# Optimization experiments

Hardware: AMD Instinct MI355X
Metric: run time of the kernel (lower is better)

The kernel has to match this reference:

```python
import jax, jax.numpy as jnp
import numpy as np

B, T, D = 32, 4096, 512  # batch, encoder timesteps t_k, attn_sz (== encoder dim == state_sz)


def setup_inputs() -> dict:
    key = jax.random.key(0)
    ks = jax.random.split(key, 7)
    scale = 1.0 / np.sqrt(D)
    return {
        "h_i": jax.random.normal(ks[0], (B, T, D), dtype=jnp.float32),
        "s_t": jax.random.normal(ks[1], (B, D), dtype=jnp.float32),
        "coverage": jax.random.uniform(ks[2], (B, T), dtype=jnp.float32),
        "W_h": jax.random.normal(ks[3], (D, D), dtype=jnp.float32) * scale,
        "W_s": jax.random.normal(ks[4], (D, D), dtype=jnp.float32) * scale,
        "b_s": jnp.zeros((D,), dtype=jnp.float32),
        "W_c": jax.random.normal(ks[5], (1, D), dtype=jnp.float32) * scale,
        "V": jax.random.normal(ks[6], (D, 1), dtype=jnp.float32) * scale,
    }


def reference(h_i, s_t, coverage, W_h, W_s, b_s, W_c, V):
    # enc_features: (B, T, D)
    enc_features = jnp.einsum("btd,de->bte", h_i, W_h)
    # dec_features: (B, D) broadcast over T
    dec_features = s_t @ W_s + b_s
    # coverage term: Dense(D) applied to coverage[..., None] -> outer product with W_c row
    cov_features = coverage[..., None] * W_c[0]  # (B, T, D)
    features = enc_features + dec_features[:, None, :] + cov_features
    # e_t = V(tanh(features)) squeezed to (B, T)
    e_t = jnp.einsum("bte,e->bt", jnp.tanh(features), V[:, 0])
    a_t = jax.nn.softmax(e_t, axis=1)  # (B, T)
    new_coverage = coverage + a_t
    # context = a_t^T h_i : (B, D)
    context_vector = jnp.einsum("bt,btd->bd", a_t, h_i)
    return context_vector, a_t, new_coverage
```

## Files before the change

### kernel.cpp

```cpp
#include <hip/hip_runtime.h>
#include <stdint.h>

#define B_ 32
#define T_ 4096
#define D_ 512
#define BT_ (B_*T_)

typedef __attribute__((ext_vector_type(8))) short bf16x8;
typedef __attribute__((ext_vector_type(4))) float f32x4;

__device__ __forceinline__ unsigned short f2bf(float f) {
    unsigned int u = __float_as_uint(f);
    u += 0x7FFFu + ((u >> 16) & 1u);
    return (unsigned short)(u >> 16);
}

__device__ __forceinline__ float tanh_fast(float x) {
    float e2 = __expf(2.0f * x);
    return 1.0f - 2.0f / (e2 + 1.0f);
}

__global__ __launch_bounds__(256) void k_conv_wh(const float* __restrict__ W_h,
                                                 unsigned short* __restrict__ wsb) {
    int tid = blockIdx.x * 256 + threadIdx.x;
    int l  = tid & 63;
    int kt = (tid >> 6) & 15;
    int nt = tid >> 10;
    int n  = nt * 16 + (l & 15);
    int k0 = kt * 32 + (l >> 4) * 8;
    unsigned int w[4];
#pragma unroll
    for (int q = 0; q < 4; ++q) {
        unsigned short lo = f2bf(W_h[(size_t)(k0 + 2*q)     * D_ + n]);
        unsigned short hi = f2bf(W_h[(size_t)(k0 + 2*q + 1) * D_ + n]);
        w[q] = (unsigned int)lo | ((unsigned int)hi << 16);
    }
    uint4 pk = {w[0], w[1], w[2], w[3]};
    ((uint4*)wsb)[tid] = pk;
}

__global__ __launch_bounds__(256) void k_dec(const float* __restrict__ s_t,
                                             const float* __restrict__ W_s,
                                             const float* __restrict__ b_s,
                                             float* __restrict__ dec) {
    int b = blockIdx.x;
    int c = threadIdx.x;
    float a0 = b_s[c], a1 = b_s[c + 256];
    const float* srow = s_t + b * D_;
    for (int k = 0; k < D_; ++k) {
        float s = srow[k];
        const float* wr = W_s + (size_t)k * D_;
        a0 = fmaf(s, wr[c], a0);
        a1 = fmaf(s, wr[c + 256], a1);
    }
    dec[b * D_ + c] = a0;
    dec[b * D_ + c + 256] = a1;
}

__global__ __launch_bounds__(512, 4) void k_main(const float* __restrict__ h_i,
                                                 const float* __restrict__ coverage,
                                                 const unsigned short* __restrict__ wsb,
                                                 const float* __restrict__ dec,
                                                 const float* __restrict__ W_c,
                                                 const float* __restrict__ V,
                                                 float* __restrict__ e_out,
                                                 float* __restrict__ part) {
    __shared__ __align__(16) unsigned char As[65536];
    __shared__ float red[8][64];
    __shared__ float wexp[64];
    const int tid = threadIdx.x;
    const int w = tid >> 6, l = tid & 63;
    const int row0 = blockIdx.x * 64;
    const int b    = row0 >> 12;
    const int t0   = row0 & (T_ - 1);

    float4 L0[8], L1[8];
#pragma unroll
    for (int i = 0; i < 8; ++i) {
        const float* src = h_i + (size_t)(row0 + i * 8 + w) * D_ + l * 8;
        L0[i] = *(const float4*)(src);
        L1[i] = *(const float4*)(src + 4);
    }
    {
        const int kt   = l >> 2;
        const int lam  = 16 * (l & 3);
        const int sl_m = (l & 3) << 1;
#pragma unroll
        for (int i = 0; i < 8; ++i) {
            int row = i * 8 + w;
            uint4 pk;
            pk.x = (unsigned)f2bf(L0[i].x) | ((unsigned)f2bf(L0[i].y) << 16);
            pk.y = (unsigned)f2bf(L0[i].z) | ((unsigned)f2bf(L0[i].w) << 16);
            pk.z = (unsigned)f2bf(L1[i].x) | ((unsigned)f2bf(L1[i].y) << 16);
            pk.w = (unsigned)f2bf(L1[i].z) | ((unsigned)f2bf(L1[i].w) << 16);
            int lamf = lam + (row & 15);
            int slot = (lamf & 0x38) | ((lamf & 7) ^ sl_m ^ (kt & 1));
            int byte = (((row >> 4) * 16 + kt) << 10) + (slot << 4);
            *(uint4*)(As + byte) = pk;
        }
    }
    __syncthreads();

    const int slotR = (l & 0x38) | ((l & 7) ^ (((l >> 4) & 3) << 1));

    f32x4 acc[4][4];
#pragma unroll
    for (int af = 0; af < 4; ++af)
#pragma unroll
        for (int j = 0; j < 4; ++j) acc[af][j] = (f32x4){0, 0, 0, 0};

    const uint4* bw = (const uint4*)wsb + ((w * 4) << 10) + l;

    {
        uint4 bp[2][4];
#pragma unroll
        for (int j = 0; j < 4; ++j) bp[0][j] = bw[(j << 10)];
#pragma unroll
        for (int j = 0; j < 4; ++j) bp[1][j] = bw[(j << 10) + (1 << 6)];
#pragma unroll
        for (int kt = 0; kt < 16; ++kt) {
            const int sl = ((slotR ^ (kt & 1)) << 4);
#pragma unroll
            for (int af = 0; af < 4; ++af) {
                uint4 araw = *(const uint4*)(As + ((af * 16 + kt) << 10) + sl);
                bf16x8 a = __builtin_bit_cast(bf16x8, araw);
#pragma unroll
                for (int j = 0; j < 4; ++j) {
                    bf16x8 bv = __builtin_bit_cast(bf16x8, bp[kt & 1][j]);
                    acc[af][j] = __builtin_amdgcn_mfma_f32_16x16x32_bf16(a, bv, acc[af][j], 0, 0, 0);
                }
            }
            if (kt < 14) {
#pragma unroll
                for (int j = 0; j < 4; ++j)
                    bp[kt & 1][j] = bw[(j << 10) + ((kt + 2) << 6)];
            }
        }
    }

    const int rgrp = (l >> 4) * 4;
    float cov_r[4][4];
#pragma unroll
    for (int af = 0; af < 4; ++af)
#pragma unroll
        for (int r = 0; r < 4; ++r)
            cov_r[af][r] = coverage[b * T_ + t0 + af * 16 + rgrp + r];

    float p[4][4] = {{0,0,0,0},{0,0,0,0},{0,0,0,0},{0,0,0,0}};
#pragma unroll
    for (int j = 0; j < 4; ++j) {
        int col = w * 64 + j * 16 + (l & 15);
        float dv = dec[b * D_ + col];
        float wc = W_c[col];
        float vv = V[col];
#pragma unroll
        for (int af = 0; af < 4; ++af)
#pragma unroll
            for (int r = 0; r < 4; ++r) {
                float x = acc[af][j][r] + dv + cov_r[af][r] * wc;
                p[af][r] += tanh_fast(x) * vv;
            }
    }

#pragma unroll
    for (int m = 1; m <= 8; m <<= 1)
#pragma unroll
        for (int af = 0; af < 4; ++af)
#pragma unroll
            for (int r = 0; r < 4; ++r)
                p[af][r] += __shfl_xor(p[af][r], m, 64);
    if ((l & 15) == 0) {
#pragma unroll
        for (int af = 0; af < 4; ++af)
#pragma unroll
            for (int r = 0; r < 4; ++r)
                red[w][af * 16 + rgrp + r] = p[af][r];
    }
    __syncthreads();
    if (tid < 64) {
        float e = red[0][tid] + red[1][tid] + red[2][tid] + red[3][tid]
                + red[4][tid] + red[5][tid] + red[6][tid] + red[7][tid];
        e_out[b * T_ + t0 + tid] = e;
        wexp[tid] = __expf(e);
    }
    __syncthreads();

    {
        const int d    = tid;
        const int ktg  = d >> 5;
        const int mq   = (d >> 3) & 3;
        const int base2 = ((mq << 4) | (((mq << 1) ^ (ktg & 1)) & 7)) << 4;
        const unsigned char* Ag = As + (ktg << 10) + ((d & 7) << 1);
        float cacc = 0.f;
#pragma unroll
        for (int t = 0; t < 64; ++t) {
            int byte = ((t >> 4) << 14) + (base2 ^ ((t & 15) << 4));
            unsigned short u = *(const unsigned short*)(Ag + byte);
            float hv = __uint_as_float(((unsigned)u) << 16);
            cacc = fmaf(wexp[t], hv, cacc);
        }
        part[(size_t)blockIdx.x * D_ + d] = cacc;
    }
}

__global__ __launch_bounds__(256) void k_soft(const float* __restrict__ e_in,
                                              const float* __restrict__ coverage,
                                              float* __restrict__ out_at,
                                              float* __restrict__ out_cov,
                                              float* __restrict__ Sb) {
    int b = blockIdx.x, tid = threadIdx.x;
    __shared__ float red[4];
    float v[16];
    float m = -1e30f;
#pragma unroll
    for (int i = 0; i < 16; ++i) {
        v[i] = e_in[b * T_ + tid + i * 256];
        m = fmaxf(m, v[i]);
    }
#pragma unroll
    for (int mk = 1; mk <= 32; mk <<= 1) m = fmaxf(m, __shfl_xor(m, mk, 64));
    if ((tid & 63) == 0) red[tid >> 6] = m;
    __syncthreads();
    m = fmaxf(fmaxf(red[0], red[1]), fmaxf(red[2], red[3]));
    float s = 0.f;
#pragma unroll
    for (int i = 0; i < 16; ++i) { v[i] = expf(v[i] - m); s += v[i]; }
#pragma unroll
    for (int mk = 1; mk <= 32; mk <<= 1) s += __shfl_xor(s, mk, 64);
    __syncthreads();
    if ((tid & 63) == 0) red[tid >> 6] = s;
    __syncthreads();
    s = red[0] + red[1] + red[2] + red[3];
    if (tid == 0) Sb[b] = __expf(m) * s;
    float inv = 1.0f / s;
#pragma unroll
    for (int i = 0; i < 16; ++i) {
        int idx = b * T_ + tid + i * 256;
        float a = v[i] * inv;
        out_at[idx]  = a;
        out_cov[idx] = coverage[idx] + a;
    }
}

__global__ __launch_bounds__(256) void k_comb(const float* __restrict__ part,
                                              const float* __restrict__ Sb,
                                              float* __restrict__ out_ctx) {
    int idx = blockIdx.x * 256 + threadIdx.x;
    int b = idx >> 9, d = idx & 511;
    const float* pp = part + (size_t)b * 64 * D_ + d;
    float s = 0.f;
#pragma unroll 8
    for (int j = 0; j < 64; ++j) s += pp[(size_t)j * D_];
    out_ctx[idx] = s / Sb[b];
}

extern "C" void kernel_launch(void* const* d_in, const int* in_sizes, int n_in,
                              void* d_out, int out_size, void* d_ws, size_t ws_size,
                              hipStream_t stream) {
    const float* h_i      = (const float*)d_in[0];
    const float* s_t      = (const float*)d_in[1];
    const float* coverage = (const float*)d_in[2];
    const float* W_h      = (const float*)d_in[3];
    const float* W_s      = (const float*)d_in[4];
    const float* b_s      = (const float*)d_in[5];
    const float* W_c      = (const float*)d_in[6];
    const float* V        = (const float*)d_in[7];

    float* out_ctx = (float*)d_out;
    float* out_at  = out_ctx + B_ * D_;
    float* out_cov = out_at + BT_;

    unsigned short* wsb = (unsigned short*)d_ws;
    float* dec  = (float*)((char*)d_ws + 524288);
    float* part = dec + B_ * D_;
    float* Sb   = part + (size_t)BT_ / 64 * D_;

    k_conv_wh<<<128, 256, 0, stream>>>(W_h, wsb);
    k_dec<<<B_, 256, 0, stream>>>(s_t, W_s, b_s, dec);
    k_main<<<BT_ / 64, 512, 0, stream>>>(h_i, coverage, wsb, dec, W_c, V, out_at, part);
    k_soft<<<B_, 256, 0, stream>>>(out_at, coverage, out_at, out_cov, Sb);
    k_comb<<<B_ * D_ / 256, 256, 0, stream>>>(part, Sb, out_ctx);
}
```

Measured before the change: 168.4 us.

## Pipeline h_i staging into LDS across K-chunks overlapped with MFMA loop

Before, each block loaded its whole 64x512 h_i tile into registers, converted it to bf16 and stored it to LDS before any MFMA work began. Now each thread stages one 64-column chunk (two k-tiles) per iteration, with global loads issued two chunks ahead. Conversion and the LDS store of the next chunk are interleaved with the MFMA work on the current chunk, so the global-load latency can hide behind compute. The cost is seven extra workgroup barriers inside the K loop and scheduling pinned in place with sched_barrier. Live registers drop from 16 float4s to 4.

New measurement: 312.5 us. 85.6% more time.

```diff
diff --git a/kernel.cpp b/kernel.cpp
--- a/kernel.cpp
+++ b/kernel.cpp
@@ -74,67 +74,105 @@
     const int b    = row0 >> 12;
     const int t0   = row0 & (T_ - 1);
 
-    float4 L0[8], L1[8];
-#pragma unroll
-    for (int i = 0; i < 8; ++i) {
-        const float* src = h_i + (size_t)(row0 + i * 8 + w) * D_ + l * 8;
-        L0[i] = *(const float4*)(src);
-        L1[i] = *(const float4*)(src + 4);
+    const int srow = tid >> 3;
+    const int t8   = tid & 7;
+    const int ktb  = (t8 >> 2) & 1;
+    const int m    = t8 & 3;
+    const int lamf = (srow & 15) + 16 * m;
+    const int slot = (lamf & 0x38) | ((lamf & 7) ^ (m << 1) ^ ktb);
+    const int sbyte0 = ((((srow >> 4) * 16) + ktb) << 10) | (slot << 4);
+    const float* gsrc = h_i + (size_t)(row0 + srow) * D_ + t8 * 8;
+
+    float4 L[2][2];
+#pragma unroll
+    for (int p = 0; p < 2; ++p) {
+        L[p][0] = *(const float4*)(gsrc + p * 64);
+        L[p][1] = *(const float4*)(gsrc + p * 64 + 4);
     }
     {
-        const int kt   = l >> 2;
-        const int lam  = 16 * (l & 3);
-        const int sl_m = (l & 3) << 1;
-#pragma unroll
-        for (int i = 0; i < 8; ++i) {
-            int row = i * 8 + w;
-            uint4 pk;
-            pk.x = (unsigned)f2bf(L0[i].x) | ((unsigned)f2bf(L0[i].y) << 16);
-            pk.y = (unsigned)f2bf(L0[i].z) | ((unsigned)f2bf(L0[i].w) << 16);
-            pk.z = (unsigned)f2bf(L1[i].x) | ((unsigned)f2bf(L1[i].y) << 16);
-            pk.w = (unsigned)f2bf(L1[i].z) | ((unsigned)f2bf(L1[i].w) << 16);
-            int lamf = lam + (row & 15);
-            int slot = (lamf & 0x38) | ((lamf & 7) ^ sl_m ^ (kt & 1));
-            int byte = (((row >> 4) * 16 + kt) << 10) + (slot << 4);
-            *(uint4*)(As + byte) = pk;
-        }
-    }
-    __syncthreads();
+        uint4 pk;
+        pk.x = (unsigned)f2bf(L[0][0].x) | ((unsigned)f2bf(L[0][0].y) << 16);
+        pk.y = (unsigned)f2bf(L[0][0].z) | ((unsigned)f2bf(L[0][0].w) << 16);
+        pk.z = (unsigned)f2bf(L[0][1].x) | ((unsigned)f2bf(L[0][1].y) << 16);
+        pk.w = (unsigned)f2bf(L[0][1].z) | ((unsigned)f2bf(L[0][1].w) << 16);
+        *(uint4*)(As + sbyte0) = pk;
+    }
+    asm volatile("s_waitcnt lgkmcnt(0)" ::: "memory");
+    __builtin_amdgcn_s_barrier();
 
     const int slotR = (l & 0x38) | ((l & 7) ^ (((l >> 4) & 3) << 1));
+    const uint4* bw = (const uint4*)wsb + ((w * 4) << 10) + l;
 
     f32x4 acc[4][4];
 #pragma unroll
     for (int af = 0; af < 4; ++af)
 #pragma unroll
-        for (int j = 0; j < 4; ++j) acc[af][j] = (f32x4){0, 0, 0, 0};
-
-    const uint4* bw = (const uint4*)wsb + ((w * 4) << 10) + l;
-
-    {
-        uint4 bp[2][4];
-#pragma unroll
-        for (int j = 0; j < 4; ++j) bp[0][j] = bw[(j << 10)];
-#pragma unroll
-        for (int j = 0; j < 4; ++j) bp[1][j] = bw[(j << 10) + (1 << 6)];
-#pragma unroll
-        for (int kt = 0; kt < 16; ++kt) {
-            const int sl = ((slotR ^ (kt & 1)) << 4);
+        for (int jj = 0; jj < 4; ++jj) acc[af][jj] = (f32x4){0, 0, 0, 0};
+
+    uint4 bq0[4], bq1[4];
+#pragma unroll
+    for (int jj = 0; jj < 4; ++jj) bq0[jj] = bw[(jj << 10)];
+#pragma unroll
+    for (int jj = 0; jj < 4; ++jj) bq1[jj] = bw[(jj << 10) + (1 << 6)];
+
+#pragma unroll
+    for (int j = 0; j < 8; ++j) {
+        if (j + 2 < 8) {
+            L[j & 1][0] = *(const float4*)(gsrc + (j + 2) * 64);
+            L[j & 1][1] = *(const float4*)(gsrc + (j + 2) * 64 + 4);
+        }
+        __builtin_amdgcn_sched_barrier(0);
+
+        {
+            const int kt = 2 * j;
+            const int sl = (slotR ^ (kt & 1)) << 4;
 #pragma unroll
             for (int af = 0; af < 4; ++af) {
                 uint4 araw = *(const uint4*)(As + ((af * 16 + kt) << 10) + sl);
                 bf16x8 a = __builtin_bit_cast(bf16x8, araw);
 #pragma unroll
-                for (int j = 0; j < 4; ++j) {
-                    bf16x8 bv = __builtin_bit_cast(bf16x8, bp[kt & 1][j]);
-                    acc[af][j] = __builtin_amdgcn_mfma_f32_16x16x32_bf16(a, bv, acc[af][j], 0, 0, 0);
+                for (int jj = 0; jj < 4; ++jj) {
+                    bf16x8 bv = __builtin_bit_cast(bf16x8, bq0[jj]);
+                    acc[af][jj] = __builtin_amdgcn_mfma_f32_16x16x32_bf16(a, bv, acc[af][jj], 0, 0, 0);
                 }
             }
-            if (kt < 14) {
-#pragma unroll
-                for (int j = 0; j < 4; ++j)
-                    bp[kt & 1][j] = bw[(j << 10) + ((kt + 2) << 6)];
-            }
+            if (j < 7) {
+#pragma unroll
+                for (int jj = 0; jj < 4; ++jj) bq0[jj] = bw[(jj << 10) + ((2 * j + 2) << 6)];
+            }
+        }
+        {
+            const int kt = 2 * j + 1;
+            const int sl = (slotR ^ (kt & 1)) << 4;
+#pragma unroll
+            for (int af = 0; af < 4; ++af) {
+                uint4 araw = *(const uint4*)(As + ((af * 16 + kt) << 10) + sl);
+                bf16x8 a = __builtin_bit_cast(bf16x8, araw);
+#pragma unroll
+                for (int jj = 0; jj < 4; ++jj) {
+                    bf16x8 bv = __builtin_bit_cast(bf16x8, bq1[jj]);
+                    acc[af][jj] = __builtin_amdgcn_mfma_f32_16x16x32_bf16(a, bv, acc[af][jj], 0, 0, 0);
+                }
+            }
+            if (j < 7) {
+#pragma unroll
+                for (int jj = 0; jj < 4; ++jj) bq1[jj] = bw[(jj << 10) + ((2 * j + 3) << 6)];
+            }
+        }
+        __builtin_amdgcn_sched_barrier(0);
+
+        if (j + 1 < 8) {
+            float4* Lp = L[(j + 1) & 1];
+            uint4 pk;
+            pk.x = (unsigned)f2bf(Lp[0].x) | ((unsigned)f2bf(Lp[0].y) << 16);
+            pk.y = (unsigned)f2bf(Lp[0].z) | ((unsigned)f2bf(Lp[0].w) << 16);
+            pk.z = (unsigned)f2bf(Lp[1].x) | ((unsigned)f2bf(Lp[1].y) << 16);
+            pk.w = (unsigned)f2bf(Lp[1].z) | ((unsigned)f2bf(Lp[1].w) << 16);
+            *(uint4*)(As + sbyte0 + ((2 * (j + 1)) << 10)) = pk;
+        }
+        if (j < 7) {
+            asm volatile("s_waitcnt lgkmcnt(0)" ::: "memory");
+            __builtin_amdgcn_s_barrier();
         }
     }
 
@@ -148,8 +186,8 @@
 
     float p[4][4] = {{0,0,0,0},{0,0,0,0},{0,0,0,0},{0,0,0,0}};
 #pragma unroll
-    for (int j = 0; j < 4; ++j) {
-        int col = w * 64 + j * 16 + (l & 15);
+    for (int jj = 0; jj < 4; ++jj) {
+        int col = w * 64 + jj * 16 + (l & 15);
         float dv = dec[b * D_ + col];
         float wc = W_c[col];
         float vv = V[col];
@@ -157,18 +195,18 @@
         for (int af = 0; af < 4; ++af)
 #pragma unroll
             for (int r = 0; r < 4; ++r) {
-                float x = acc[af][j][r] + dv + cov_r[af][r] * wc;
+                float x = acc[af][jj][r] + dv + cov_r[af][r] * wc;
                 p[af][r] += tanh_fast(x) * vv;
             }
     }
 
 #pragma unroll
-    for (int m = 1; m <= 8; m <<= 1)
+    for (int mm = 1; mm <= 8; mm <<= 1)
 #pragma unroll
         for (int af = 0; af < 4; ++af)
 #pragma unroll
             for (int r = 0; r < 4; ++r)
-                p[af][r] += __shfl_xor(p[af][r], m, 64);
+                p[af][r] += __shfl_xor(p[af][r], mm, 64);
     if ((l & 15) == 0) {
 #pragma unroll
         for (int af = 0; af < 4; ++af)
```

## Stream h_i tile into LDS as fp32 via async global_load_lds pipeline

Applied to the files above, without the earlier changes.

The main kernel now copies the fp32 h_i tile straight into LDS with global_load_lds in four stages. Each quarter's MFMA work starts as soon as its stage lands (vmcnt waits plus barriers), and bf16 conversion moves to the point where LDS is read. The context reduction now reads fp32 h_i from LDS and reduces across lanes with shuffles, which also removes the earlier rounding of h_i to bf16 in the context. In exchange the LDS footprint doubles to 128KB, so occupancy falls (launch bounds lowered to 2) and conversion work repeats inside the MFMA loop.

Measured after the change: 237.2 us. +40.8%, slower.

```diff
diff --git a/kernel.cpp b/kernel.cpp
--- a/kernel.cpp
+++ b/kernel.cpp
@@ -15,10 +15,22 @@
     return (unsigned short)(u >> 16);
 }
 
+__device__ __forceinline__ unsigned pk2(float a, float b) {
+    return (unsigned)f2bf(a) | ((unsigned)f2bf(b) << 16);
+}
+
 __device__ __forceinline__ float tanh_fast(float x) {
     float e2 = __expf(2.0f * x);
     return 1.0f - 2.0f / (e2 + 1.0f);
 }
+
+__device__ __forceinline__ void gl16(const float* g, const float* lds) {
+    __builtin_amdgcn_global_load_lds(
+        (const __attribute__((address_space(1))) void*)g,
+        (__attribute__((address_space(3))) void*)lds, 16, 0, 0);
+}
+
+#define WAITVM(N) asm volatile("s_waitcnt vmcnt(" #N ")" ::: "memory")
 
 __global__ __launch_bounds__(256) void k_conv_wh(const float* __restrict__ W_h,
                                                  unsigned short* __restrict__ wsb) {
@@ -57,7 +69,7 @@
     dec[b * D_ + c + 256] = a1;
 }
 
-__global__ __launch_bounds__(512, 4) void k_main(const float* __restrict__ h_i,
+__global__ __launch_bounds__(512, 2) void k_main(const float* __restrict__ h_i,
                                                  const float* __restrict__ coverage,
                                                  const unsigned short* __restrict__ wsb,
                                                  const float* __restrict__ dec,
@@ -65,7 +77,7 @@
                                                  const float* __restrict__ V,
                                                  float* __restrict__ e_out,
                                                  float* __restrict__ part) {
-    __shared__ __align__(16) unsigned char As[65536];
+    __shared__ __align__(16) float As[64 * 512];
     __shared__ float red[8][64];
     __shared__ float wexp[64];
     const int tid = threadIdx.x;
@@ -74,71 +86,93 @@
     const int b    = row0 >> 12;
     const int t0   = row0 & (T_ - 1);
 
-    float4 L0[8], L1[8];
-#pragma unroll
-    for (int i = 0; i < 8; ++i) {
-        const float* src = h_i + (size_t)(row0 + i * 8 + w) * D_ + l * 8;
-        L0[i] = *(const float4*)(src);
-        L1[i] = *(const float4*)(src + 4);
-    }
-    {
-        const int kt   = l >> 2;
-        const int lam  = 16 * (l & 3);
-        const int sl_m = (l & 3) << 1;
-#pragma unroll
-        for (int i = 0; i < 8; ++i) {
-            int row = i * 8 + w;
-            uint4 pk;
-            pk.x = (unsigned)f2bf(L0[i].x) | ((unsigned)f2bf(L0[i].y) << 16);
-            pk.y = (unsigned)f2bf(L0[i].z) | ((unsigned)f2bf(L0[i].w) << 16);
-            pk.z = (unsigned)f2bf(L1[i].x) | ((unsigned)f2bf(L1[i].y) << 16);
-            pk.w = (unsigned)f2bf(L1[i].z) | ((unsigned)f2bf(L1[i].w) << 16);
-            int lamf = lam + (row & 15);
-            int slot = (lamf & 0x38) | ((lamf & 7) ^ sl_m ^ (kt & 1));
-            int byte = (((row >> 4) * 16 + kt) << 10) + (slot << 4);
-            *(uint4*)(As + byte) = pk;
-        }
-    }
-    __syncthreads();
-
-    const int slotR = (l & 0x38) | ((l & 7) ^ (((l >> 4) & 3) << 1));
+    const float* gp = h_i + (size_t)(row0 + (w >> 1) * 16 + (l & 15)) * D_
+                          + ((l >> 4) * 8) + (w & 1) * 64;
+    const float* lb = As + ((w >> 1) * 16 + (w & 1) * 2) * 512;
+
+#define STG(Q, II) gl16(gp + ((Q)*128 + ((II)>>1)*32 + ((II)&1)*4), \
+                        lb + ((Q)*4 + ((II)>>1))*512 + ((II)&1)*256)
+
+    STG(0,0); STG(0,1); STG(0,2); STG(0,3);
+    STG(1,0); STG(1,1); STG(1,2); STG(1,3);
+    STG(2,0); STG(2,1); STG(2,2); STG(2,3);
+
+    const int rgrp = (l >> 4) * 4;
+    const uint4* bw = (const uint4*)wsb + ((w * 4) << 10) + l;
 
     f32x4 acc[4][4];
 #pragma unroll
     for (int af = 0; af < 4; ++af)
 #pragma unroll
-        for (int j = 0; j < 4; ++j) acc[af][j] = (f32x4){0, 0, 0, 0};
-
-    const uint4* bw = (const uint4*)wsb + ((w * 4) << 10) + l;
-
-    {
-        uint4 bp[2][4];
-#pragma unroll
-        for (int j = 0; j < 4; ++j) bp[0][j] = bw[(j << 10)];
-#pragma unroll
-        for (int j = 0; j < 4; ++j) bp[1][j] = bw[(j << 10) + (1 << 6)];
-#pragma unroll
-        for (int kt = 0; kt < 16; ++kt) {
-            const int sl = ((slotR ^ (kt & 1)) << 4);
-#pragma unroll
-            for (int af = 0; af < 4; ++af) {
-                uint4 araw = *(const uint4*)(As + ((af * 16 + kt) << 10) + sl);
-                bf16x8 a = __builtin_bit_cast(bf16x8, araw);
-#pragma unroll
-                for (int j = 0; j < 4; ++j) {
-                    bf16x8 bv = __builtin_bit_cast(bf16x8, bp[kt & 1][j]);
-                    acc[af][j] = __builtin_amdgcn_mfma_f32_16x16x32_bf16(a, bv, acc[af][j], 0, 0, 0);
-                }
-            }
-            if (kt < 14) {
-#pragma unroll
-                for (int j = 0; j < 4; ++j)
-                    bp[kt & 1][j] = bw[(j << 10) + ((kt + 2) << 6)];
-            }
-        }
-    }
-
-    const int rgrp = (l >> 4) * 4;
+        for (int jj = 0; jj < 4; ++jj) acc[af][jj] = (f32x4){0, 0, 0, 0};
+
+#define QMM(Q)                                                                \
+    _Pragma("unroll")                                                         \
+    for (int ktl = 0; ktl < 4; ++ktl) {                                       \
+        _Pragma("unroll")                                                     \
+        for (int af = 0; af < 4; ++af) {                                      \
+            const float* fr = As + (af * 16 + (Q) * 4 + ktl) * 512 + l * 4;   \
+            float4 lo = *(const float4*)fr;                                   \
+            float4 hi = *(const float4*)(fr + 256);                           \
+            uint4 a4 = {pk2(lo.x, lo.y), pk2(lo.z, lo.w),                     \
+                        pk2(hi.x, hi.y), pk2(hi.z, hi.w)};                    \
+            bf16x8 a = __builtin_bit_cast(bf16x8, a4);                        \
+            _Pragma("unroll")                                                 \
+            for (int jj = 0; jj < 4; ++jj)                                    \
+                acc[af][jj] = __builtin_amdgcn_mfma_f32_16x16x32_bf16(        \
+                    a, __builtin_bit_cast(bf16x8, bq[ktl][jj]),               \
+                    acc[af][jj], 0, 0, 0);                                    \
+        }                                                                     \
+    }
+
+#define BLOADS(Q)                                                             \
+    _Pragma("unroll")                                                         \
+    for (int ktl = 0; ktl < 4; ++ktl)                                         \
+        _Pragma("unroll")                                                     \
+        for (int jj = 0; jj < 4; ++jj)                                        \
+            bq[ktl][jj] = bw[(jj << 10) + (((Q) * 4 + ktl) << 6)];
+
+    WAITVM(8);
+    __builtin_amdgcn_s_barrier();
+    __builtin_amdgcn_sched_barrier(0);
+    {
+        uint4 bq[4][4];
+        BLOADS(0);
+        __builtin_amdgcn_sched_barrier(0);
+        STG(3,0); STG(3,1);
+        __builtin_amdgcn_sched_barrier(0);
+        QMM(0);
+    }
+    WAITVM(6);
+    __builtin_amdgcn_s_barrier();
+    __builtin_amdgcn_sched_barrier(0);
+    {
+        uint4 bq[4][4];
+        BLOADS(1);
+        __builtin_amdgcn_sched_barrier(0);
+        STG(3,2); STG(3,3);
+        __builtin_amdgcn_sched_barrier(0);
+        QMM(1);
+    }
+    WAITVM(4);
+    __builtin_amdgcn_s_barrier();
+    __builtin_amdgcn_sched_barrier(0);
+    {
+        uint4 bq[4][4];
+        BLOADS(2);
+        __builtin_amdgcn_sched_barrier(0);
+        QMM(2);
+    }
+    WAITVM(0);
+    __builtin_amdgcn_s_barrier();
+    __builtin_amdgcn_sched_barrier(0);
+    {
+        uint4 bq[4][4];
+        BLOADS(3);
+        __builtin_amdgcn_sched_barrier(0);
+        QMM(3);
+    }
+
     float cov_r[4][4];
 #pragma unroll
     for (int af = 0; af < 4; ++af)
@@ -148,8 +182,8 @@
 
     float p[4][4] = {{0,0,0,0},{0,0,0,0},{0,0,0,0},{0,0,0,0}};
 #pragma unroll
-    for (int j = 0; j < 4; ++j) {
-        int col = w * 64 + j * 16 + (l & 15);
+    for (int jj = 0; jj < 4; ++jj) {
+        int col = w * 64 + jj * 16 + (l & 15);
         float dv = dec[b * D_ + col];
         float wc = W_c[col];
         float vv = V[col];
@@ -157,18 +191,18 @@
         for (int af = 0; af < 4; ++af)
 #pragma unroll
             for (int r = 0; r < 4; ++r) {
-                float x = acc[af][j][r] + dv + cov_r[af][r] * wc;
+                float x = acc[af][jj][r] + dv + cov_r[af][r] * wc;
                 p[af][r] += tanh_fast(x) * vv;
             }
     }
 
 #pragma unroll
-    for (int m = 1; m <= 8; m <<= 1)
+    for (int mm = 1; mm <= 8; mm <<= 1)
 #pragma unroll
         for (int af = 0; af < 4; ++af)
 #pragma unroll
             for (int r = 0; r < 4; ++r)
-                p[af][r] += __shfl_xor(p[af][r], m, 64);
+                p[af][r] += __shfl_xor(p[af][r], mm, 64);
     if ((l & 15) == 0) {
 #pragma unroll
         for (int af = 0; af < 4; ++af)
@@ -186,20 +220,42 @@
     __syncthreads();
 
     {
-        const int d    = tid;
-        const int ktg  = d >> 5;
-        const int mq   = (d >> 3) & 3;
-        const int base2 = ((mq << 4) | (((mq << 1) ^ (ktg & 1)) & 7)) << 4;
-        const unsigned char* Ag = As + (ktg << 10) + ((d & 7) << 1);
-        float cacc = 0.f;
-#pragma unroll
-        for (int t = 0; t < 64; ++t) {
-            int byte = ((t >> 4) << 14) + (base2 ^ ((t & 15) << 4));
-            unsigned short u = *(const unsigned short*)(Ag + byte);
-            float hv = __uint_as_float(((unsigned)u) << 16);
-            cacc = fmaf(wexp[t], hv, cacc);
+        float pc[2][8] = {{0,0,0,0,0,0,0,0},{0,0,0,0,0,0,0,0}};
+#pragma unroll
+        for (int ktq = 0; ktq < 2; ++ktq) {
+            const int kt = w * 2 + ktq;
+#pragma unroll
+            for (int af = 0; af < 4; ++af) {
+                float wv = wexp[af * 16 + (l & 15)];
+                const float* fr = As + (af * 16 + kt) * 512 + l * 4;
+                float4 lo = *(const float4*)fr;
+                float4 hi = *(const float4*)(fr + 256);
+                pc[ktq][0] = fmaf(wv, lo.x, pc[ktq][0]);
+                pc[ktq][1] = fmaf(wv, lo.y, pc[ktq][1]);
+                pc[ktq][2] = fmaf(wv, lo.z, pc[ktq][2]);
+                pc[ktq][3] = fmaf(wv, lo.w, pc[ktq][3]);
+                pc[ktq][4] = fmaf(wv, hi.x, pc[ktq][4]);
+                pc[ktq][5] = fmaf(wv, hi.y, pc[ktq][5]);
+                pc[ktq][6] = fmaf(wv, hi.z, pc[ktq][6]);
+                pc[ktq][7] = fmaf(wv, hi.w, pc[ktq][7]);
+            }
         }
-        part[(size_t)blockIdx.x * D_ + d] = cacc;
+#pragma unroll
+        for (int mm = 1; mm <= 8; mm <<= 1)
+#pragma unroll
+            for (int ktq = 0; ktq < 2; ++ktq)
+#pragma unroll
+                for (int j = 0; j < 8; ++j)
+                    pc[ktq][j] += __shfl_xor(pc[ktq][j], mm, 64);
+        if ((l & 15) == 0) {
+#pragma unroll
+            for (int ktq = 0; ktq < 2; ++ktq) {
+                float* dst = part + (size_t)blockIdx.x * D_
+                           + (w * 2 + ktq) * 32 + (l >> 4) * 8;
+                *(float4*)dst       = float4{pc[ktq][0], pc[ktq][1], pc[ktq][2], pc[ktq][3]};
+                *(float4*)(dst + 4) = float4{pc[ktq][4], pc[ktq][5], pc[ktq][6], pc[ktq][7]};
+            }
+        }
     }
 }
 
```

## Double k_main block to 1024 threads with 16 waves splitting N columns

Applied to the files above, without the earlier changes.

k_main now launches 1024 threads (16 waves) per 64-row tile, so each wave computes 32 output columns instead of 64. That halves per-thread accumulators and B-fragment registers and is meant to raise latency hiding. The h_i load is split into two passes of fewer registers. The context partial sum is restructured so each lane reads a 16-byte bf16 row chunk and reduces with cross-lane shuffles instead of scalar 2-byte LDS reads. The cost is that each wave loads a slice of W_h per block, and the larger blocks may limit occupancy, given 64KB of LDS per block and launch bounds of (1024, 8).

Result: slower. 212.6 us (+26.3%).

```diff
diff --git a/kernel.cpp b/kernel.cpp
--- a/kernel.cpp
+++ b/kernel.cpp
@@ -13,6 +13,10 @@
     unsigned int u = __float_as_uint(f);
     u += 0x7FFFu + ((u >> 16) & 1u);
     return (unsigned short)(u >> 16);
+}
+
+__device__ __forceinline__ unsigned pk2(float a, float b) {
+    return (unsigned)f2bf(a) | ((unsigned)f2bf(b) << 16);
 }
 
 __device__ __forceinline__ float tanh_fast(float x) {
@@ -57,16 +61,16 @@
     dec[b * D_ + c + 256] = a1;
 }
 
-__global__ __launch_bounds__(512, 4) void k_main(const float* __restrict__ h_i,
-                                                 const float* __restrict__ coverage,
-                                                 const unsigned short* __restrict__ wsb,
-                                                 const float* __restrict__ dec,
-                                                 const float* __restrict__ W_c,
-                                                 const float* __restrict__ V,
-                                                 float* __restrict__ e_out,
-                                                 float* __restrict__ part) {
+__global__ __launch_bounds__(1024, 8) void k_main(const float* __restrict__ h_i,
+                                                  const float* __restrict__ coverage,
+                                                  const unsigned short* __restrict__ wsb,
+                                                  const float* __restrict__ dec,
+                                                  const float* __restrict__ W_c,
+                                                  const float* __restrict__ V,
+                                                  float* __restrict__ e_out,
+                                                  float* __restrict__ part) {
     __shared__ __align__(16) unsigned char As[65536];
-    __shared__ float red[8][64];
+    __shared__ float red[16][64];
     __shared__ float wexp[64];
     const int tid = threadIdx.x;
     const int w = tid >> 6, l = tid & 63;
@@ -74,101 +78,92 @@
     const int b    = row0 >> 12;
     const int t0   = row0 & (T_ - 1);
 
-    float4 L0[8], L1[8];
-#pragma unroll
-    for (int i = 0; i < 8; ++i) {
-        const float* src = h_i + (size_t)(row0 + i * 8 + w) * D_ + l * 8;
-        L0[i] = *(const float4*)(src);
-        L1[i] = *(const float4*)(src + 4);
-    }
+    const int kt_s = l >> 2;
+    const int lamf = ((l & 3) << 4) + w;
+    const int slot = (lamf & 0x38) | ((lamf & 7) ^ (((l & 3) << 1)) ^ (kt_s & 1));
+    const int sb0  = (kt_s << 10) + (slot << 4);
+    const float* gsrc = h_i + (size_t)(row0 + w) * D_ + l * 8;
+
+#pragma unroll
+    for (int pass = 0; pass < 2; ++pass) {
+        float4 Lf[2][2];
+#pragma unroll
+        for (int i = 0; i < 2; ++i) {
+            const float* src = gsrc + (size_t)((pass * 2 + i) * 16) * D_;
+            Lf[i][0] = *(const float4*)src;
+            Lf[i][1] = *(const float4*)(src + 4);
+        }
+#pragma unroll
+        for (int i = 0; i < 2; ++i) {
+            uint4 pk;
+            pk.x = pk2(Lf[i][0].x, Lf[i][0].y);
+            pk.y = pk2(Lf[i][0].z, Lf[i][0].w);
+            pk.z = pk2(Lf[i][1].x, Lf[i][1].y);
+            pk.w = pk2(Lf[i][1].z, Lf[i][1].w);
+            *(uint4*)(As + (((pass * 2 + i) * 16) << 10) + sb0) = pk;
+        }
+    }
+    __syncthreads();
+
+    const int slotR = (l & 0x38) | ((l & 7) ^ (((l >> 4) & 3) << 1));
+    const uint4* bw = (const uint4*)wsb + ((w * 2) << 10) + l;
+
+    f32x4 acc[4][2];
+#pragma unroll
+    for (int af = 0; af < 4; ++af) {
+        acc[af][0] = (f32x4){0, 0, 0, 0};
+        acc[af][1] = (f32x4){0, 0, 0, 0};
+    }
+    uint4 bp[2][2];
+    bp[0][0] = bw[0];        bp[0][1] = bw[1 << 10];
+    bp[1][0] = bw[1 << 6];   bp[1][1] = bw[(1 << 10) + (1 << 6)];
+
+#pragma unroll
+    for (int kt = 0; kt < 16; ++kt) {
+        const int sl = (slotR ^ (kt & 1)) << 4;
+#pragma unroll
+        for (int af = 0; af < 4; ++af) {
+            uint4 araw = *(const uint4*)(As + ((af * 16 + kt) << 10) + sl);
+            bf16x8 a = __builtin_bit_cast(bf16x8, araw);
+            acc[af][0] = __builtin_amdgcn_mfma_f32_16x16x32_bf16(
+                a, __builtin_bit_cast(bf16x8, bp[kt & 1][0]), acc[af][0], 0, 0, 0);
+            acc[af][1] = __builtin_amdgcn_mfma_f32_16x16x32_bf16(
+                a, __builtin_bit_cast(bf16x8, bp[kt & 1][1]), acc[af][1], 0, 0, 0);
+        }
+        if (kt < 14) {
+            bp[kt & 1][0] = bw[((kt + 2) << 6)];
+            bp[kt & 1][1] = bw[(1 << 10) + ((kt + 2) << 6)];
+        }
+    }
+
+    const int rgrp = (l >> 4) * 4;
+    float p[4][4] = {{0,0,0,0},{0,0,0,0},{0,0,0,0},{0,0,0,0}};
     {
-        const int kt   = l >> 2;
-        const int lam  = 16 * (l & 3);
-        const int sl_m = (l & 3) << 1;
-#pragma unroll
-        for (int i = 0; i < 8; ++i) {
-            int row = i * 8 + w;
-            uint4 pk;
-            pk.x = (unsigned)f2bf(L0[i].x) | ((unsigned)f2bf(L0[i].y) << 16);
-            pk.y = (unsigned)f2bf(L0[i].z) | ((unsigned)f2bf(L0[i].w) << 16);
-            pk.z = (unsigned)f2bf(L1[i].x) | ((unsigned)f2bf(L1[i].y) << 16);
-            pk.w = (unsigned)f2bf(L1[i].z) | ((unsigned)f2bf(L1[i].w) << 16);
-            int lamf = lam + (row & 15);
-            int slot = (lamf & 0x38) | ((lamf & 7) ^ sl_m ^ (kt & 1));
-            int byte = (((row >> 4) * 16 + kt) << 10) + (slot << 4);
-            *(uint4*)(As + byte) = pk;
-        }
-    }
-    __syncthreads();
-
-    const int slotR = (l & 0x38) | ((l & 7) ^ (((l >> 4) & 3) << 1));
-
-    f32x4 acc[4][4];
-#pragma unroll
-    for (int af = 0; af < 4; ++af)
-#pragma unroll
-        for (int j = 0; j < 4; ++j) acc[af][j] = (f32x4){0, 0, 0, 0};
-
-    const uint4* bw = (const uint4*)wsb + ((w * 4) << 10) + l;
-
-    {
-        uint4 bp[2][4];
-#pragma unroll
-        for (int j = 0; j < 4; ++j) bp[0][j] = bw[(j << 10)];
-#pragma unroll
-        for (int j = 0; j < 4; ++j) bp[1][j] = bw[(j << 10) + (1 << 6)];
-#pragma unroll
-        for (int kt = 0; kt < 16; ++kt) {
-            const int sl = ((slotR ^ (kt & 1)) << 4);
-#pragma unroll
-            for (int af = 0; af < 4; ++af) {
-                uint4 araw = *(const uint4*)(As + ((af * 16 + kt) << 10) + sl);
-                bf16x8 a = __builtin_bit_cast(bf16x8, araw);
-#pragma unroll
-                for (int j = 0; j < 4; ++j) {
-                    bf16x8 bv = __builtin_bit_cast(bf16x8, bp[kt & 1][j]);
-                    acc[af][j] = __builtin_amdgcn_mfma_f32_16x16x32_bf16(a, bv, acc[af][j], 0, 0, 0);
-                }
+        int col0 = w * 32 + (l & 15);
+        float dv0 = dec[b * D_ + col0],      wc0 = W_c[col0],      vv0 = V[col0];
+        float dv1 = dec[b * D_ + col0 + 16], wc1 = W_c[col0 + 16], vv1 = V[col0 + 16];
+#pragma unroll
+        for (int af = 0; af < 4; ++af) {
+            float cov_r[4];
+#pragma unroll
+            for (int r = 0; r < 4; ++r)
+                cov_r[r] = coverage[b * T_ + t0 + af * 16 + rgrp + r];
+#pragma unroll
+            for (int r = 0; r < 4; ++r) {
+                float x0 = acc[af][0][r] + dv0 + cov_r[r] * wc0;
+                float x1 = acc[af][1][r] + dv1 + cov_r[r] * wc1;
+                p[af][r] += tanh_fast(x0) * vv0 + tanh_fast(x1) * vv1;
             }
-            if (kt < 14) {
-#pragma unroll
-                for (int j = 0; j < 4; ++j)
-                    bp[kt & 1][j] = bw[(j << 10) + ((kt + 2) << 6)];
-            }
-        }
-    }
-
-    const int rgrp = (l >> 4) * 4;
-    float cov_r[4][4];
-#pragma unroll
-    for (int af = 0; af < 4; ++af)
-#pragma unroll
-        for (int r = 0; r < 4; ++r)
-            cov_r[af][r] = coverage[b * T_ + t0 + af * 16 + rgrp + r];
-
-    float p[4][4] = {{0,0,0,0},{0,0,0,0},{0,0,0,0},{0,0,0,0}};
-#pragma unroll
-    for (int j = 0; j < 4; ++j) {
-        int col = w * 64 + j * 16 + (l & 15);
-        float dv = dec[b * D_ + col];
-        float wc = W_c[col];
-        float vv = V[col];
+        }
+    }
+
+#pragma unroll
+    for (int mm = 1; mm <= 8; mm <<= 1)
 #pragma unroll
         for (int af = 0; af < 4; ++af)
 #pragma unroll
-            for (int r = 0; r < 4; ++r) {
-                float x = acc[af][j][r] + dv + cov_r[af][r] * wc;
-                p[af][r] += tanh_fast(x) * vv;
-            }
-    }
-
-#pragma unroll
-    for (int m = 1; m <= 8; m <<= 1)
-#pragma unroll
-        for (int af = 0; af < 4; ++af)
-#pragma unroll
             for (int r = 0; r < 4; ++r)
-                p[af][r] += __shfl_xor(p[af][r], m, 64);
+                p[af][r] += __shfl_xor(p[af][r], mm, 64);
     if ((l & 15) == 0) {
 #pragma unroll
         for (int af = 0; af < 4; ++af)
@@ -178,28 +173,40 @@
     }
     __syncthreads();
     if (tid < 64) {
-        float e = red[0][tid] + red[1][tid] + red[2][tid] + red[3][tid]
-                + red[4][tid] + red[5][tid] + red[6][tid] + red[7][tid];
+        float e = 0.f;
+#pragma unroll
+        for (int ww = 0; ww < 16; ++ww) e += red[ww][tid];
         e_out[b * T_ + t0 + tid] = e;
         wexp[tid] = __expf(e);
     }
     __syncthreads();
 
     {
-        const int d    = tid;
-        const int ktg  = d >> 5;
-        const int mq   = (d >> 3) & 3;
-        const int base2 = ((mq << 4) | (((mq << 1) ^ (ktg & 1)) & 7)) << 4;
-        const unsigned char* Ag = As + (ktg << 10) + ((d & 7) << 1);
-        float cacc = 0.f;
-#pragma unroll
-        for (int t = 0; t < 64; ++t) {
-            int byte = ((t >> 4) << 14) + (base2 ^ ((t & 15) << 4));
-            unsigned short u = *(const unsigned short*)(Ag + byte);
-            float hv = __uint_as_float(((unsigned)u) << 16);
-            cacc = fmaf(wexp[t], hv, cacc);
-        }
-        part[(size_t)blockIdx.x * D_ + d] = cacc;
+        float pc[8] = {0, 0, 0, 0, 0, 0, 0, 0};
+        const int sl = (slotR ^ (w & 1)) << 4;
+#pragma unroll
+        for (int af = 0; af < 4; ++af) {
+            float wv = wexp[af * 16 + (l & 15)];
+            uint4 araw = *(const uint4*)(As + ((af * 16 + w) << 10) + sl);
+            const unsigned* u = (const unsigned*)&araw;
+#pragma unroll
+            for (int q = 0; q < 4; ++q) {
+                float f0 = __uint_as_float(u[q] << 16);
+                float f1 = __uint_as_float(u[q] & 0xffff0000u);
+                pc[2 * q]     = fmaf(wv, f0, pc[2 * q]);
+                pc[2 * q + 1] = fmaf(wv, f1, pc[2 * q + 1]);
+            }
+        }
+#pragma unroll
+        for (int mm = 1; mm <= 8; mm <<= 1)
+#pragma unroll
+            for (int j = 0; j < 8; ++j)
+                pc[j] += __shfl_xor(pc[j], mm, 64);
+        if ((l & 15) == 0) {
+            float* dst = part + (size_t)blockIdx.x * D_ + w * 32 + (l >> 4) * 8;
+            *(float4*)dst       = float4{pc[0], pc[1], pc[2], pc[3]};
+            *(float4*)(dst + 4) = float4{pc[4], pc[5], pc[6], pc[7]};
+        }
     }
 }
 
@@ -277,7 +284,7 @@
 
     k_conv_wh<<<128, 256, 0, stream>>>(W_h, wsb);
     k_dec<<<B_, 256, 0, stream>>>(s_t, W_s, b_s, dec);
-    k_main<<<BT_ / 64, 512, 0, stream>>>(h_i, coverage, wsb, dec, W_c, V, out_at, part);
+    k_main<<<BT_ / 64, 1024, 0, stream>>>(h_i, coverage, wsb, dec, W_c, V, out_at, part);
     k_soft<<<B_, 256, 0, stream>>>(out_at, coverage, out_at, out_cov, Sb);
     k_comb<<<B_ * D_ / 256, 256, 0, stream>>>(part, Sb, out_ctx);
 }
```
